# Kernel tuning notes

Hardware: AMD Instinct MI355X
Metric: run time of the kernel (lower is better)

## Reference

```python
import jax, jax.numpy as jnp
import numpy as np

N_NODES = 100000
N_EDGES = 1600000
IN_C = 256
H1 = 128
H2 = 64
OUT_C = 64


def setup_inputs() -> dict:
    key = jax.random.key(0)
    ks = jax.random.split(key, 8)
    x = jax.random.normal(ks[0], (N_NODES, IN_C), dtype=jnp.float32)
    edge_src = jax.random.randint(ks[1], (N_EDGES,), 0, N_NODES, dtype=jnp.int32)
    edge_dst = jax.random.randint(ks[2], (N_EDGES,), 0, N_NODES, dtype=jnp.int32)
    edge_weight = jax.random.uniform(ks[3], (N_EDGES,), dtype=jnp.float32)
    W1 = jax.random.normal(ks[4], (IN_C, H1), dtype=jnp.float32) / np.sqrt(IN_C)
    b1 = jnp.zeros((H1,), dtype=jnp.float32)
    W2 = jax.random.normal(ks[5], (H1, H2), dtype=jnp.float32) / np.sqrt(H1)
    b2 = jnp.zeros((H2,), dtype=jnp.float32)
    W3 = jax.random.normal(ks[6], (H2, OUT_C), dtype=jnp.float32) / np.sqrt(H2)
    b3 = jnp.zeros((OUT_C,), dtype=jnp.float32)
    return dict(x=x, edge_src=edge_src, edge_dst=edge_dst, edge_weight=edge_weight,
                W1=W1, b1=b1, W2=W2, b2=b2, W3=W3, b3=b3)


def _gcn_layer(h, W, b, src, dst, ew):
    # GraphConvolution: out = adj @ (h @ W) + b, adj given as weighted edge list
    support = h @ W                      # [N, d_out] dense GEMM
    msg = support[src] * ew[:, None]     # [E, d_out] gather (irregular access)
    agg = jax.ops.segment_sum(msg, dst, num_segments=N_NODES)  # SpMM scatter-add
    return agg + b


def reference(x, edge_src, edge_dst, edge_weight, W1, b1, W2, b2, W3, b3):
    # Eval-mode forward: dropout is identity (training=False)
    h = jax.nn.relu(_gcn_layer(x, W1, b1, edge_src, edge_dst, edge_weight))
    h = jax.nn.relu(_gcn_layer(h, W2, b2, edge_src, edge_dst, edge_weight))
    out = _gcn_layer(h, W3, b3, edge_src, edge_dst, edge_weight)
    return out
```

## Files before the change

### kernel.cpp

```cpp
#include <hip/hip_runtime.h>
#include <hip/hip_bf16.h>


__device__ __forceinline__ unsigned short f2bf(float f) {
    unsigned int u = __float_as_uint(f);
    unsigned int r = (u + 0x7fffu + ((u >> 16) & 1u)) >> 16;
    return (unsigned short)r;
}

using frag_ab = __attribute__((ext_vector_type(8))) short;
using frag_cd = __attribute__((ext_vector_type(4))) float;

template <int BN>
__global__ __launch_bounds__(256) void mfma_gemm_kernel(
    const float* __restrict__ A, const unsigned short* __restrict__ WT,
    unsigned short* __restrict__ C, int M, int K)
{
    constexpr int BM = 64, BK = 64;
    constexpr int LDA = BK + 8;
    __shared__ unsigned short As[BM * LDA];
    __shared__ unsigned short Bs[BN * LDA];

    const int tid = threadIdx.x;
    const int wave = tid >> 6;
    const int lane = tid & 63;
    const int quad = lane >> 4;
    const int l16 = lane & 15;
    const int m0 = blockIdx.x * BM;

    frag_cd acc[BN / 16];
#pragma unroll
    for (int f = 0; f < BN / 16; ++f) acc[f] = (frag_cd){0.f, 0.f, 0.f, 0.f};

    for (int k0 = 0; k0 < K; k0 += BK) {
#pragma unroll
        for (int i = 0; i < 4; ++i) {
            const int linear = (i * 256 + tid) * 4;
            const int r = linear >> 6;
            const int c = linear & 63;
            const int row = m0 + r;
            float4 v = make_float4(0.f, 0.f, 0.f, 0.f);
            if (row < M) v = *(const float4*)&A[(size_t)row * K + k0 + c];
            ushort4 u;
            u.x = f2bf(v.x); u.y = f2bf(v.y); u.z = f2bf(v.z); u.w = f2bf(v.w);
            *(ushort4*)&As[r * LDA + c] = u;
        }
#pragma unroll
        for (int i = 0; i < BN / 32; ++i) {
            const int linear = (i * 256 + tid) * 8;
            const int n = linear >> 6;
            const int c = linear & 63;
            const uint4 u = *(const uint4*)&WT[(size_t)n * K + k0 + c];
            *(uint4*)&Bs[n * LDA + c] = u;
        }
        __syncthreads();

#pragma unroll
        for (int ks = 0; ks < 2; ++ks) {
            const int kk = ks * 32 + quad * 8;
            const frag_ab a = *(const frag_ab*)&As[(wave * 16 + l16) * LDA + kk];
#pragma unroll
            for (int f = 0; f < BN / 16; ++f) {
                const frag_ab b = *(const frag_ab*)&Bs[(f * 16 + l16) * LDA + kk];
                acc[f] = __builtin_amdgcn_mfma_f32_16x16x32_bf16(a, b, acc[f], 0, 0, 0);
            }
        }
        __syncthreads();
    }

#pragma unroll
    for (int f = 0; f < BN / 16; ++f) {
#pragma unroll
        for (int r = 0; r < 4; ++r) {
            const int row = m0 + wave * 16 + quad * 4 + r;
            if (row < M) C[(size_t)row * BN + f * 16 + l16] = f2bf(acc[f][r]);
        }
    }
}

__global__ __launch_bounds__(256) void wt_kernel(
    const float* __restrict__ W1, const float* __restrict__ W2, const float* __restrict__ W3,
    unsigned short* __restrict__ WT1, unsigned short* __restrict__ WT2, unsigned short* __restrict__ WT3)
{
    const int i = blockIdx.x * 256 + threadIdx.x;
    const float* W; unsigned short* WT; int K, N, j;
    if (i < 32768)      { W = W1; WT = WT1; K = 256; N = 128; j = i; }
    else if (i < 40960) { W = W2; WT = WT2; K = 128; N = 64;  j = i - 32768; }
    else if (i < 45056) { W = W3; WT = WT3; K = 64;  N = 64;  j = i - 40960; }
    else return;
    const int n = j / K, k = j % K;
    WT[j] = f2bf(W[k * N + n]);
}

__global__ __launch_bounds__(256) void zero_int_kernel(int* __restrict__ p, int n)
{
    const int i = blockIdx.x * 256 + threadIdx.x;
    if (i < n) p[i] = 0;
}

__global__ __launch_bounds__(256) void hist_kernel(
    const int* __restrict__ dst, int* __restrict__ deg, int E)
{
    const int e = blockIdx.x * 256 + threadIdx.x;
    if (e < E) atomicAdd(&deg[dst[e]], 1);
}

__global__ __launch_bounds__(256) void scan1_kernel(
    const int* __restrict__ deg, int* __restrict__ offs, int* __restrict__ bsum, int n)
{
    __shared__ int tmp[256];
    const int i = blockIdx.x * 256 + threadIdx.x;
    const int v = (i < n) ? deg[i] : 0;
    tmp[threadIdx.x] = v;
    __syncthreads();
#pragma unroll
    for (int d = 1; d < 256; d <<= 1) {
        const int t = (threadIdx.x >= d) ? tmp[threadIdx.x - d] : 0;
        __syncthreads();
        tmp[threadIdx.x] += t;
        __syncthreads();
    }
    if (i < n) offs[i] = tmp[threadIdx.x] - v;
    if (threadIdx.x == 255) bsum[blockIdx.x] = tmp[255];
}

__global__ __launch_bounds__(512) void scan2_kernel(int* __restrict__ bsum, int nb)
{
    __shared__ int tmp[512];
    const int v = ((int)threadIdx.x < nb) ? bsum[threadIdx.x] : 0;
    tmp[threadIdx.x] = v;
    __syncthreads();
#pragma unroll
    for (int d = 1; d < 512; d <<= 1) {
        const int t = ((int)threadIdx.x >= d) ? tmp[threadIdx.x - d] : 0;
        __syncthreads();
        tmp[threadIdx.x] += t;
        __syncthreads();
    }
    if ((int)threadIdx.x < nb) bsum[threadIdx.x] = tmp[threadIdx.x] - v;
}

__global__ __launch_bounds__(256) void scan3_kernel(
    int* __restrict__ offs, const int* __restrict__ bsum, int* __restrict__ cursor,
    int n, int E)
{
    const int i = blockIdx.x * 256 + threadIdx.x;
    if (i < n) {
        const int o = offs[i] + bsum[blockIdx.x];
        offs[i] = o;
        cursor[i] = o;
    }
    if (i == 0) offs[n] = E;
}

__global__ __launch_bounds__(256) void fill_kernel(
    const int* __restrict__ src, const int* __restrict__ dst, const float* __restrict__ ew,
    int* __restrict__ cursor, uint2* __restrict__ ecsr, int E)
{
    const int e = blockIdx.x * 256 + threadIdx.x;
    if (e >= E) return;
    const int pos = atomicAdd(&cursor[dst[e]], 1);
    ecsr[pos] = make_uint2((unsigned)src[e], __float_as_uint(ew[e]));
}

template <int D, int LOGT, bool RELU>
__global__ __launch_bounds__(256) void gather_agg_kernel(
    const unsigned short* __restrict__ S, const int* __restrict__ offs,
    const uint2* __restrict__ ecsr,
    const float* __restrict__ bias, float* __restrict__ out, int N)
{
    const int TPN = 1 << LOGT;
    const int gid = blockIdx.x * 256 + threadIdx.x;
    const int node = gid >> LOGT;
    if (node >= N) return;
    const int lane = gid & (TPN - 1);
    const int c8 = lane << 3;

    const int j0 = offs[node];
    const int j1 = offs[node + 1];

    float acc[8];
#pragma unroll
    for (int c = 0; c < 8; ++c) acc[c] = 0.f;

    for (int jb = j0; jb < j1; jb += TPN) {
        const int j = jb + lane;
        int myc = 0;
        float myw = 0.f;
        if (j < j1) {
            const uint2 p = ecsr[j];
            myc = (int)p.x;
            myw = __uint_as_float(p.y);
        }
        const int cnt = min(TPN, j1 - jb);
        for (int t = 0; t < cnt; ++t) {
            const int s = __shfl(myc, t, TPN);
            const float w = __shfl(myw, t, TPN);
            const uint4 v = *(const uint4*)&S[(size_t)s * D + c8];
#pragma unroll
            for (int q = 0; q < 4; ++q) {
                const unsigned int u = (&v.x)[q];
                const float lo = __uint_as_float(u << 16);
                const float hi = __uint_as_float(u & 0xffff0000u);
                acc[q * 2 + 0] += w * lo;
                acc[q * 2 + 1] += w * hi;
            }
        }
    }

#pragma unroll
    for (int c = 0; c < 8; ++c) {
        float v = acc[c] + bias[c8 + c];
        if (RELU) v = fmaxf(v, 0.f);
        acc[c] = v;
    }
    float4* op = (float4*)&out[(size_t)node * D + c8];
    op[0] = make_float4(acc[0], acc[1], acc[2], acc[3]);
    op[1] = make_float4(acc[4], acc[5], acc[6], acc[7]);
}

extern "C" void kernel_launch(void* const* d_in, const int* in_sizes, int n_in,
                              void* d_out, int out_size, void* d_ws, size_t ws_size,
                              hipStream_t stream)
{
    const float* x    = (const float*)d_in[0];
    const int*   esrc = (const int*)  d_in[1];
    const int*   edst = (const int*)  d_in[2];
    const float* ew   = (const float*)d_in[3];
    const float* W1   = (const float*)d_in[4];
    const float* b1   = (const float*)d_in[5];
    const float* W2   = (const float*)d_in[6];
    const float* b2   = (const float*)d_in[7];
    const float* W3   = (const float*)d_in[8];
    const float* b3   = (const float*)d_in[9];

    const int N = in_sizes[0] / 256;
    const int E = in_sizes[1];

    unsigned short* Sb = (unsigned short*)d_ws;
    float* H   = (float*)(Sb + (size_t)N * 128);
    unsigned short* WT1 = (unsigned short*)(H + (size_t)N * 128);
    unsigned short* WT2 = WT1 + 256 * 128;
    unsigned short* WT3 = WT2 + 128 * 64;
    uint2* ecsr = (uint2*)(WT3 + 64 * 64);
    int* deg    = (int*)(ecsr + E);
    int* offs   = deg + N;
    int* cursor = offs + N + 4;
    int* bsum   = cursor + N;
    float* out  = (float*)d_out;

    const dim3 blk(256);
    const int nblkN = (N + 255) / 256;
    const int nblkE = (E + 255) / 256;
    const int mblocks = (N + 63) / 64;

    wt_kernel<<<(45056 + 255) / 256, blk, 0, stream>>>(W1, W2, W3, WT1, WT2, WT3);
    zero_int_kernel<<<nblkN, blk, 0, stream>>>(deg, N);
    hist_kernel<<<nblkE, blk, 0, stream>>>(edst, deg, E);
    scan1_kernel<<<nblkN, blk, 0, stream>>>(deg, offs, bsum, N);
    scan2_kernel<<<1, 512, 0, stream>>>(bsum, nblkN);
    scan3_kernel<<<nblkN, blk, 0, stream>>>(offs, bsum, cursor, N, E);
    fill_kernel<<<nblkE, blk, 0, stream>>>(esrc, edst, ew, cursor, ecsr, E);

    mfma_gemm_kernel<128><<<mblocks, blk, 0, stream>>>(x, WT1, Sb, N, 256);
    gather_agg_kernel<128, 4, true><<<((N * 16) + 255) / 256, blk, 0, stream>>>(
        Sb, offs, ecsr, b1, H, N);

    mfma_gemm_kernel<64><<<mblocks, blk, 0, stream>>>(H, WT2, Sb, N, 128);
    gather_agg_kernel<64, 3, true><<<((N * 8) + 255) / 256, blk, 0, stream>>>(
        Sb, offs, ecsr, b2, H, N);

    mfma_gemm_kernel<64><<<mblocks, blk, 0, stream>>>(H, WT3, Sb, N, 64);
    gather_agg_kernel<64, 3, false><<<((N * 8) + 255) / 256, blk, 0, stream>>>(
        Sb, offs, ecsr, b3, out, N);
}
```

Baseline: 542.8 us.

## Build CSR with two-pass bucketed counting sort instead of global atomic fill

```diff
diff --git a/kernel.cpp b/kernel.cpp
--- a/kernel.cpp
+++ b/kernel.cpp
@@ -1,6 +1,8 @@
 #include <hip/hip_runtime.h>
 #include <hip/hip_bf16.h>
 
+
+#define EPB 8192
 
 __device__ __forceinline__ unsigned short f2bf(float f) {
     unsigned int u = __float_as_uint(f);
@@ -141,26 +143,116 @@
 }
 
 __global__ __launch_bounds__(256) void scan3_kernel(
-    int* __restrict__ offs, const int* __restrict__ bsum, int* __restrict__ cursor,
-    int n, int E)
-{
-    const int i = blockIdx.x * 256 + threadIdx.x;
-    if (i < n) {
-        const int o = offs[i] + bsum[blockIdx.x];
-        offs[i] = o;
-        cursor[i] = o;
-    }
+    int* __restrict__ offs, const int* __restrict__ bsum, int n, int E)
+{
+    const int i = blockIdx.x * 256 + threadIdx.x;
+    if (i < n) offs[i] += bsum[blockIdx.x];
     if (i == 0) offs[n] = E;
 }
 
-__global__ __launch_bounds__(256) void fill_kernel(
+__global__ __launch_bounds__(256) void count_kernel(
+    const int* __restrict__ dst, int* __restrict__ cmat, int E, int nblk, int nbuck)
+{
+    __shared__ int hist[1600];
+    for (int i = threadIdx.x; i < nbuck; i += 256) hist[i] = 0;
+    __syncthreads();
+    const int base = blockIdx.x * EPB;
+    const int end = min(base + EPB, E);
+    for (int e = base + threadIdx.x; e < end; e += 256)
+        atomicAdd(&hist[dst[e] >> 6], 1);
+    __syncthreads();
+    for (int i = threadIdx.x; i < nbuck; i += 256)
+        cmat[(size_t)i * nblk + blockIdx.x] = hist[i];
+}
+
+__global__ __launch_bounds__(256) void scanA_kernel(
+    int* __restrict__ data, int* __restrict__ psum, int L)
+{
+    __shared__ int tmp[256];
+    const int b0 = blockIdx.x * 1024 + threadIdx.x * 4;
+    int v[4] = {0, 0, 0, 0};
+    if (b0 + 3 < L) { const int4 t = *(const int4*)&data[b0]; v[0]=t.x; v[1]=t.y; v[2]=t.z; v[3]=t.w; }
+    else { for (int i = 0; i < 4; ++i) if (b0 + i < L) v[i] = data[b0 + i]; }
+    const int s = v[0] + v[1] + v[2] + v[3];
+    tmp[threadIdx.x] = s;
+    __syncthreads();
+#pragma unroll
+    for (int d = 1; d < 256; d <<= 1) {
+        const int t = (threadIdx.x >= d) ? tmp[threadIdx.x - d] : 0;
+        __syncthreads();
+        tmp[threadIdx.x] += t;
+        __syncthreads();
+    }
+    int run = tmp[threadIdx.x] - s;
+    int o[4];
+#pragma unroll
+    for (int i = 0; i < 4; ++i) { o[i] = run; run += v[i]; }
+    if (b0 + 3 < L) { *(int4*)&data[b0] = make_int4(o[0], o[1], o[2], o[3]); }
+    else { for (int i = 0; i < 4; ++i) if (b0 + i < L) data[b0 + i] = o[i]; }
+    if (threadIdx.x == 255) psum[blockIdx.x] = tmp[255];
+}
+
+__global__ __launch_bounds__(1024) void scanB_kernel(int* __restrict__ psum, int nb)
+{
+    __shared__ int tmp[1024];
+    const int v = ((int)threadIdx.x < nb) ? psum[threadIdx.x] : 0;
+    tmp[threadIdx.x] = v;
+    __syncthreads();
+#pragma unroll
+    for (int d = 1; d < 1024; d <<= 1) {
+        const int t = ((int)threadIdx.x >= d) ? tmp[threadIdx.x - d] : 0;
+        __syncthreads();
+        tmp[threadIdx.x] += t;
+        __syncthreads();
+    }
+    if ((int)threadIdx.x < nb) psum[threadIdx.x] = tmp[threadIdx.x] - v;
+}
+
+__global__ __launch_bounds__(256) void scanC_kernel(
+    int* __restrict__ data, const int* __restrict__ psum, int L)
+{
+    const int i = blockIdx.x * 256 + threadIdx.x;
+    if (i < L) data[i] += psum[i >> 10];
+}
+
+__global__ __launch_bounds__(256) void place_kernel(
     const int* __restrict__ src, const int* __restrict__ dst, const float* __restrict__ ew,
-    int* __restrict__ cursor, uint2* __restrict__ ecsr, int E)
-{
-    const int e = blockIdx.x * 256 + threadIdx.x;
-    if (e >= E) return;
-    const int pos = atomicAdd(&cursor[dst[e]], 1);
-    ecsr[pos] = make_uint2((unsigned)src[e], __float_as_uint(ew[e]));
+    const int* __restrict__ cmat, uint2* __restrict__ ebuck, int E, int nblk, int nbuck)
+{
+    __shared__ int cursor[1600];
+    const int k = blockIdx.x;
+    for (int i = threadIdx.x; i < nbuck; i += 256)
+        cursor[i] = cmat[(size_t)i * nblk + k];
+    __syncthreads();
+    const int base = k * EPB;
+    const int end = min(base + EPB, E);
+    for (int e = base + threadIdx.x; e < end; e += 256) {
+        const int d = dst[e];
+        const int b = d >> 6;
+        const int pos = atomicAdd(&cursor[b], 1);
+        ebuck[pos] = make_uint2(((unsigned)src[e] << 6) | (unsigned)(d & 63),
+                                __float_as_uint(ew[e]));
+    }
+}
+
+__global__ __launch_bounds__(256) void sort2_kernel(
+    const uint2* __restrict__ ebuck, const int* __restrict__ offs,
+    uint2* __restrict__ ecsr, int N)
+{
+    __shared__ int cur[64];
+    const int b = blockIdx.x;
+    const int node0 = b << 6;
+    const int nn = min(64, N - node0);
+    if ((int)threadIdx.x < nn) cur[threadIdx.x] = offs[node0 + threadIdx.x];
+    __syncthreads();
+    const int j0 = offs[node0];
+    const int j1 = offs[node0 + nn];
+    for (int j = j0 + (int)threadIdx.x; j < j1; j += 256) {
+        const uint2 ed = ebuck[j];
+        const int dl = (int)(ed.x & 63u);
+        const int pos = atomicAdd(&cur[dl], 1);
+        ecsr[pos] = make_uint2(ed.x >> 6, ed.y);
+    }
 }
 
 template <int D, int LOGT, bool RELU>
@@ -237,16 +329,22 @@
     const int N = in_sizes[0] / 256;
     const int E = in_sizes[1];
 
+    const int nbuck = (N + 63) >> 6;
+    const int nblk = (E + EPB - 1) / EPB;
+    const int L = nbuck * nblk;
+
     unsigned short* Sb = (unsigned short*)d_ws;
     float* H   = (float*)(Sb + (size_t)N * 128);
     unsigned short* WT1 = (unsigned short*)(H + (size_t)N * 128);
     unsigned short* WT2 = WT1 + 256 * 128;
     unsigned short* WT3 = WT2 + 128 * 64;
-    uint2* ecsr = (uint2*)(WT3 + 64 * 64);
+    uint2* ebuck = (uint2*)(WT3 + 64 * 64);
+    uint2* ecsr  = ebuck + E;
     int* deg    = (int*)(ecsr + E);
     int* offs   = deg + N;
-    int* cursor = offs + N + 4;
-    int* bsum   = cursor + N;
+    int* bsum   = offs + N + 4;
+    int* cmat   = bsum + 512;
+    int* psum   = cmat + ((L + 3) & ~3);
     float* out  = (float*)d_out;
 
     const dim3 blk(256);
@@ -259,8 +357,13 @@
     hist_kernel<<<nblkE, blk, 0, stream>>>(edst, deg, E);
     scan1_kernel<<<nblkN, blk, 0, stream>>>(deg, offs, bsum, N);
     scan2_kernel<<<1, 512, 0, stream>>>(bsum, nblkN);
-    scan3_kernel<<<nblkN, blk, 0, stream>>>(offs, bsum, cursor, N, E);
-    fill_kernel<<<nblkE, blk, 0, stream>>>(esrc, edst, ew, cursor, ecsr, E);
+    scan3_kernel<<<nblkN, blk, 0, stream>>>(offs, bsum, N, E);
+    count_kernel<<<nblk, blk, 0, stream>>>(edst, cmat, E, nblk, nbuck);
+    scanA_kernel<<<(L + 1023) / 1024, blk, 0, stream>>>(cmat, psum, L);
+    scanB_kernel<<<1, 1024, 0, stream>>>(psum, (L + 1023) / 1024);
+    scanC_kernel<<<(L + 255) / 256, blk, 0, stream>>>(cmat, psum, L);
+    place_kernel<<<nblk, blk, 0, stream>>>(esrc, edst, ew, cmat, ebuck, E, nblk, nbuck);
+    sort2_kernel<<<nbuck, blk, 0, stream>>>(ebuck, offs, ecsr, N);
 
     mfma_gemm_kernel<128><<<mblocks, blk, 0, stream>>>(x, WT1, Sb, N, 256);
     gather_agg_kernel<128, 4, true><<<((N * 16) + 255) / 256, blk, 0, stream>>>(
```

New measurement: 520.3 us. 1.04x faster.
